# Kernel tuning notes

Measured on AMD Instinct MI355X. Metric: run time of the kernel, lower is better.

## Reference

```python
import jax, jax.numpy as jnp
import numpy as np

K_HOPS = 2  # SGConv K = nlayers


def setup_inputs() -> dict:
    key = jax.random.key(0)
    k1, k2, k3 = jax.random.split(key, 3)
    N, E, F, C = 100000, 1600000, 128, 40
    x = jax.random.normal(k1, (N, F), dtype=jnp.float32)
    edge_index = jax.random.randint(k2, (2, E), 0, N, dtype=jnp.int64)
    W = jax.random.normal(k3, (C, F), dtype=jnp.float32) * (1.0 / np.sqrt(F))
    b = jnp.zeros((C,), dtype=jnp.float32)
    return {"x": x, "edge_index": edge_index, "W": W, "b": b}


def reference(x, edge_index, W, b):
    # SGConv: K hops of GCN-normalized propagation (with self-loops), then Linear.
    N = x.shape[0]
    loop = jnp.arange(N, dtype=edge_index.dtype)
    src = jnp.concatenate([edge_index[0], loop])  # message source
    dst = jnp.concatenate([edge_index[1], loop])  # aggregation target
    w = jnp.ones(src.shape[0], dtype=x.dtype)     # edge_weight=None -> 1, self-loop fill=1
    deg = jax.ops.segment_sum(w, dst, num_segments=N)  # in-degree incl. self-loop (>=1)
    dinv = jax.lax.rsqrt(deg)
    norm = dinv[src] * w * dinv[dst]              # D^{-1/2} A D^{-1/2}
    h = x
    for _ in range(K_HOPS):
        h = jax.ops.segment_sum(norm[:, None] * h[src], dst, num_segments=N)
    return h @ W.T + b
```

## Files before the change

### kernel.cpp

```cpp
#include <hip/hip_runtime.h>
#include <hip/hip_fp16.h>
#include <cstdint>

#define CDIM 40
#define FDIM 128
#define BIN_SHIFT 8
#define BIN_SZ (1 << BIN_SHIFT)
#define CHUNK 4096
#define STAGE_CAP 8192

typedef _Float16 f16x8 __attribute__((ext_vector_type(8)));
typedef float f32x4 __attribute__((ext_vector_type(4)));

static __device__ __forceinline__ long long load_idx(const void* p, int is64, long long i) {
    if (is64) return ((const long long*)p)[i];
    return (long long)((const int*)p)[i];
}

static __device__ __forceinline__ unsigned packh2(float a, float b) {
    __half2 h;
    h.x = __float2half(a);
    h.y = __float2half(b);
    return *(unsigned*)&h;
}

static __device__ __forceinline__ void addv(float* acc, uint4 v) {
    const __half2* h = (const __half2*)&v;
#pragma unroll
    for (int k = 0; k < 4; ++k) {
        float2 f = __half22float2(h[k]);
        acc[2 * k]     += f.x;
        acc[2 * k + 1] += f.y;
    }
}

static __device__ __forceinline__ f16x8 cvt8(float4 a, float4 b) {
    f16x8 r;
    r[0] = (_Float16)a.x; r[1] = (_Float16)a.y; r[2] = (_Float16)a.z; r[3] = (_Float16)a.w;
    r[4] = (_Float16)b.x; r[5] = (_Float16)b.y; r[6] = (_Float16)b.z; r[7] = (_Float16)b.w;
    return r;
}

__global__ void k_init(int* cursor, int nb, int cap) {
    int i = blockIdx.x * blockDim.x + threadIdx.x;
    if (i < nb) cursor[i] = i * cap;
}

__global__ __launch_bounds__(256) void kA3(const void* ei, long long E,
                                           int nb, int* __restrict__ cursor,
                                           unsigned* __restrict__ binned) {
    __shared__ unsigned lval[CHUNK];
    __shared__ unsigned short lbin[CHUNK];
    __shared__ int lcnt[512];
    __shared__ int lbase[512];
    __shared__ int lflag;
    int tid = threadIdx.x;
    if (tid == 0) lflag = 1;
    for (int i = tid; i < nb; i += 256) lcnt[i] = 0;
    __syncthreads();
    {
        const unsigned* w = (const unsigned*)ei;
        int nscan = (int)((2 * E < 4096) ? (2 * E) : 4096);
        for (int k = 1 + 2 * tid; k < nscan; k += 512)
            if (w[k] != 0u) lflag = 0;
    }
    __syncthreads();
    int is64 = lflag;
    long long base = (long long)blockIdx.x * CHUNK;
    int nk = (int)min((long long)CHUNK, E - base);
    for (int k = tid; k < nk; k += 256) {
        long long e = base + k;
        int s = (int)load_idx(ei, is64, e);
        int d = (int)load_idx(ei, is64, E + e);
        int bin = d >> BIN_SHIFT;
        lval[k] = (unsigned)s | ((unsigned)(d & (BIN_SZ - 1)) << 17);
        lbin[k] = (unsigned short)bin;
        atomicAdd(&lcnt[bin], 1);
    }
    __syncthreads();
    for (int i = tid; i < nb; i += 256) {
        int c = lcnt[i];
        lbase[i] = c ? atomicAdd(&cursor[i], c) : 0;
        lcnt[i] = 0;
    }
    __syncthreads();
    for (int k = tid; k < nk; k += 256) {
        int bin = lbin[k];
        int loc = atomicAdd(&lcnt[bin], 1);
        binned[lbase[bin] + loc] = lval[k];
    }
}

__global__ __launch_bounds__(256) void kB(const unsigned* __restrict__ binned,
                                          const int* __restrict__ cursor, int cap,
                                          int* __restrict__ rowp, int* __restrict__ rend,
                                          float* __restrict__ dinv,
                                          int* __restrict__ perm, int* __restrict__ cursorG,
                                          int* __restrict__ csr, int N) {
    __shared__ int lcnt[BIN_SZ];
    __shared__ int lexcl[BIN_SZ];
    __shared__ int ls[256];
    __shared__ int dh[64];
    __shared__ int stage[STAGE_CAP];
    int b = blockIdx.x, tid = threadIdx.x;
    int node0 = b << BIN_SHIFT;
    int nn = min(BIN_SZ, N - node0);
    int base = b * cap;
    int nedges = cursor[b] - base;

    lcnt[tid] = 0;
    if (tid < 64) dh[tid] = 0;
    __syncthreads();
    for (int t = tid; t < nedges; t += 256)
        atomicAdd(&lcnt[(binned[base + t] >> 17) & (BIN_SZ - 1)], 1);
    __syncthreads();
    int myc = lcnt[tid];
    ls[tid] = myc;
    __syncthreads();
    for (int off = 1; off < 256; off <<= 1) {
        int t = (tid >= off) ? ls[tid - off] : 0;
        __syncthreads();
        ls[tid] += t;
        __syncthreads();
    }
    int ex = ls[tid] - myc;
    lexcl[tid] = ex;
    if (tid < nn) {
        rowp[node0 + tid] = base + ex;
        rend[node0 + tid] = base + ex + myc;
        dinv[node0 + tid] = rsqrtf(1.0f + (float)myc);
        atomicAdd(&dh[min(myc, 63)], 1);
    }
    __syncthreads();
    int dv = (tid < 64) ? dh[tid] : 0;
    ls[tid] = dv;
    __syncthreads();
    for (int off = 1; off < 64; off <<= 1) {
        int t = (tid >= off) ? ls[tid - off] : 0;
        __syncthreads();
        ls[tid] += t;
        __syncthreads();
    }
    if (tid < 64) dh[tid] = ls[tid] - dv;
    __syncthreads();
    if (tid < nn) {
        int pos = atomicAdd(&dh[min(myc, 63)], 1);
        perm[node0 + pos] = node0 + tid;
    }
    __syncthreads();
    lcnt[tid] = lexcl[tid];
    __syncthreads();
    if (nedges <= STAGE_CAP) {
        for (int t = tid; t < nedges; t += 256) {
            unsigned v = binned[base + t];
            int src = (int)(v & 0x1FFFFu);
            int dl  = (int)((v >> 17) & (BIN_SZ - 1));
            int p = atomicAdd(&lcnt[dl], 1);
            stage[p] = src;
        }
        __syncthreads();
        for (int t = tid; t < nedges; t += 256) csr[base + t] = stage[t];
    } else {
        if (tid < nn) cursorG[node0 + tid] = base + lexcl[tid];
        __syncthreads();
        for (int t = tid; t < nedges; t += 256) {
            unsigned v = binned[base + t];
            int src = (int)(v & 0x1FFFFu);
            int dl  = (int)((v >> 17) & (BIN_SZ - 1));
            int p = atomicAdd(&cursorG[node0 + dl], 1);
            csr[p] = src;
        }
    }
}

__global__ __launch_bounds__(256) void k_gemm(const float* __restrict__ x,
                                              const float* __restrict__ W,
                                              const float* __restrict__ dinv,
                                              __half* __restrict__ gA,
                                              __half* __restrict__ gB, int N) {
    int wave = threadIdx.x >> 6;
    int lane = threadIdx.x & 63;
    int m = lane & 15;
    int quad = lane >> 4;
    f16x8 bfrag[3][4];
#pragma unroll
    for (int t = 0; t < 3; ++t) {
        int c = t * 16 + m;
#pragma unroll
        for (int q = 0; q < 4; ++q) {
            if (c < CDIM) {
                const float* wp = W + (size_t)c * FDIM + q * 32 + quad * 8;
                float4 w0 = *(const float4*)wp;
                float4 w1 = *(const float4*)(wp + 4);
                bfrag[t][q] = cvt8(w0, w1);
            } else {
                f16x8 z = {0, 0, 0, 0, 0, 0, 0, 0};
                bfrag[t][q] = z;
            }
        }
    }
#pragma unroll
    for (int i = 0; i < 4; ++i) {
        int nodebase = blockIdx.x * 256 + wave * 64 + i * 16;
        if (nodebase >= N) break;
        const float* xp = x + (size_t)(nodebase + m) * FDIM + quad * 8;
        f16x8 afrag[4];
#pragma unroll
        for (int q = 0; q < 4; ++q) {
            float4 x0 = *(const float4*)(xp + q * 32);
            float4 x1 = *(const float4*)(xp + q * 32 + 4);
            afrag[q] = cvt8(x0, x1);
        }
        f32x4 acc0 = {0, 0, 0, 0}, acc1 = {0, 0, 0, 0}, acc2 = {0, 0, 0, 0};
#pragma unroll
        for (int q = 0; q < 4; ++q) {
            acc0 = __builtin_amdgcn_mfma_f32_16x16x32_f16(afrag[q], bfrag[0][q], acc0, 0, 0, 0);
            acc1 = __builtin_amdgcn_mfma_f32_16x16x32_f16(afrag[q], bfrag[1][q], acc1, 0, 0, 0);
            acc2 = __builtin_amdgcn_mfma_f32_16x16x32_f16(afrag[q], bfrag[2][q], acc2, 0, 0, 0);
        }
        float4 dvv = *(const float4*)&dinv[nodebase + quad * 4];
        float ds[4] = {dvv.x, dvv.y, dvv.z, dvv.w};
#pragma unroll
        for (int r = 0; r < 4; ++r) {
            int node = nodebase + quad * 4 + r;
            gA[(size_t)node * 32 + m]      = __float2half(acc0[r] * ds[r]);
            gA[(size_t)node * 32 + 16 + m] = __float2half(acc1[r] * ds[r]);
            if (m < 8)
                gB[(size_t)node * 8 + m]   = __float2half(acc2[r] * ds[r]);
        }
    }
}

__global__ __launch_bounds__(256) void k_gather(const int* __restrict__ rowp,
                                                const int* __restrict__ rend,
                                                const int* __restrict__ csr,
                                                const int* __restrict__ perm,
                                                const float* __restrict__ dinv,
                                                const __half* __restrict__ gA,
                                                const __half* __restrict__ gB,
                                                const float* __restrict__ b,
                                                __half* __restrict__ goA,
                                                __half* __restrict__ goB,
                                                float* __restrict__ outF,
                                                int N, int mode) {
    unsigned t = blockIdx.x * 256 + threadIdx.x;
    unsigned gidx = t / 5, c = t - gidx * 5;
    if (gidx >= (unsigned)N) return;
    int node = perm[gidx];
    const uint4* src;
    unsigned stride;
    if (c < 4) { src = (const uint4*)gA + c; stride = 4; }
    else       { src = (const uint4*)gB;     stride = 1; }
    float acc[8];
#pragma unroll
    for (int i = 0; i < 8; ++i) acc[i] = 0.0f;
    addv(acc, src[(size_t)node * stride]);
    int j = rowp[node], end = rend[node];
    for (; j + 7 < end; j += 8) {
        int s0 = csr[j], s1 = csr[j + 1], s2 = csr[j + 2], s3 = csr[j + 3];
        int s4 = csr[j + 4], s5 = csr[j + 5], s6 = csr[j + 6], s7 = csr[j + 7];
        uint4 v0 = src[(size_t)s0 * stride];
        uint4 v1 = src[(size_t)s1 * stride];
        uint4 v2 = src[(size_t)s2 * stride];
        uint4 v3 = src[(size_t)s3 * stride];
        uint4 v4 = src[(size_t)s4 * stride];
        uint4 v5 = src[(size_t)s5 * stride];
        uint4 v6 = src[(size_t)s6 * stride];
        uint4 v7 = src[(size_t)s7 * stride];
        addv(acc, v0); addv(acc, v1); addv(acc, v2); addv(acc, v3);
        addv(acc, v4); addv(acc, v5); addv(acc, v6); addv(acc, v7);
    }
    for (; j + 1 < end; j += 2) {
        int s0 = csr[j], s1 = csr[j + 1];
        uint4 v0 = src[(size_t)s0 * stride];
        uint4 v1 = src[(size_t)s1 * stride];
        addv(acc, v0); addv(acc, v1);
    }
    if (j < end) addv(acc, src[(size_t)csr[j] * stride]);
    float d = dinv[node];
    if (mode == 0) {
        float s = d * d;
        uint4 o;
        unsigned* w = (unsigned*)&o;
#pragma unroll
        for (int k = 0; k < 4; ++k)
            w[k] = packh2(acc[2 * k] * s, acc[2 * k + 1] * s);
        if (c < 4) ((uint4*)goA)[(size_t)node * 4 + c] = o;
        else       ((uint4*)goB)[node] = o;
    } else {
        const float4* b4 = (const float4*)b + 2 * c;
        float4 bv0 = b4[0], bv1 = b4[1];
        float4 o0, o1;
        o0.x = acc[0] * d + bv0.x; o0.y = acc[1] * d + bv0.y;
        o0.z = acc[2] * d + bv0.z; o0.w = acc[3] * d + bv0.w;
        o1.x = acc[4] * d + bv1.x; o1.y = acc[5] * d + bv1.y;
        o1.z = acc[6] * d + bv1.z; o1.w = acc[7] * d + bv1.w;
        float4* op = (float4*)outF + (size_t)node * 10 + 2 * c;
        op[0] = o0;
        op[1] = o1;
    }
}

static inline size_t align256(size_t v) { return (v + 255) & ~(size_t)255; }

extern "C" void kernel_launch(void* const* d_in, const int* in_sizes, int n_in,
                              void* d_out, int out_size, void* d_ws, size_t ws_size,
                              hipStream_t stream) {
    const float* x  = (const float*)d_in[0];
    const void*  ei = d_in[1];
    const float* W  = (const float*)d_in[2];
    const float* b  = (const float*)d_in[3];
    float* out = (float*)d_out;

    const int N = in_sizes[0] / FDIM;
    const long long E = (long long)in_sizes[1] / 2;

    const int nb     = (N + BIN_SZ - 1) >> BIN_SHIFT;
    const int nchunk = (int)((E + CHUNK - 1) / CHUNK);
    int cap = (int)(E / nb) + 2048;
    if (cap > STAGE_CAP) cap = STAGE_CAP;

    char* wsb = (char*)d_ws;
    size_t off = 0;
    int*      cursor  = (int*)(wsb + off);      off = align256(off + (size_t)nb * 4);
    int*      rowp    = (int*)(wsb + off);      off = align256(off + (size_t)N * 4);
    int*      rend    = (int*)(wsb + off);      off = align256(off + (size_t)N * 4);
    int*      cursorG = (int*)(wsb + off);      off = align256(off + (size_t)N * 4);
    int*      perm    = (int*)(wsb + off);      off = align256(off + (size_t)N * 4);
    float*    dinv    = (float*)(wsb + off);    off = align256(off + (size_t)N * 4);
    __half*   gA0     = (__half*)(wsb + off);   off = align256(off + (size_t)N * 32 * 2);
    __half*   gB0     = (__half*)(wsb + off);   off = align256(off + (size_t)N * 8 * 2);
    __half*   gA1     = (__half*)(wsb + off);   off = align256(off + (size_t)N * 32 * 2);
    __half*   gB1     = (__half*)(wsb + off);   off = align256(off + (size_t)N * 8 * 2);
    unsigned* binned  = (unsigned*)(wsb + off); off = align256(off + (size_t)nb * cap * 4);
    int*      csr     = (int*)(wsb + off);      off = align256(off + (size_t)nb * cap * 4);

    const int B = 256;
    const int nbGE = (N + 255) / 256;
    const unsigned GT = 5u * (unsigned)N;
    const int nbGA = (int)((GT + B - 1) / B);

    k_init  <<<(nb + 255) / 256, 256, 0, stream>>>(cursor, nb, cap);
    kA3     <<<nchunk, B, 0, stream>>>(ei, E, nb, cursor, binned);
    kB      <<<nb, B, 0, stream>>>(binned, cursor, cap, rowp, rend, dinv, perm, cursorG, csr, N);
    k_gemm  <<<nbGE, B, 0, stream>>>(x, W, dinv, gA0, gB0, N);
    k_gather<<<nbGA, B, 0, stream>>>(rowp, rend, csr, perm, dinv, gA0, gB0, b,
                                     gA1, gB1, nullptr, N, 0);
    k_gather<<<nbGA, B, 0, stream>>>(rowp, rend, csr, perm, dinv, gA1, gB1, b,
                                     nullptr, nullptr, out, N, 1);
}
```

Baseline: 222.5 us.

## Pad CSR rows to multiples of four and pack per-node gather metadata

CSR rows are padded to a multiple of four with a sentinel index pointing at an added zero row in each feature buffer. This lets the gather loop use int4 index loads with no scalar tail. The separate rowp/rend/perm/dinv arrays are replaced by one int2 meta record per degree-sorted slot, holding row start, node id and degree, and the gather recomputes dinv from the degree. The cost is some wasted gathers of the zero row and a larger CSR allocation.

After: 215.6 us. 3.1% less time.

```diff
diff --git a/kernel.cpp b/kernel.cpp
--- a/kernel.cpp
+++ b/kernel.cpp
@@ -41,9 +41,9 @@
     return r;
 }
 
-__global__ void k_init(int* cursor, int nb, int cap) {
+__global__ void k_init(int* cursor, int nb, int capRec) {
     int i = blockIdx.x * blockDim.x + threadIdx.x;
-    if (i < nb) cursor[i] = i * cap;
+    if (i < nb) cursor[i] = i * capRec;
 }
 
 __global__ __launch_bounds__(256) void kA3(const void* ei, long long E,
@@ -92,30 +92,34 @@
 }
 
 __global__ __launch_bounds__(256) void kB(const unsigned* __restrict__ binned,
-                                          const int* __restrict__ cursor, int cap,
-                                          int* __restrict__ rowp, int* __restrict__ rend,
+                                          const int* __restrict__ cursor,
+                                          int capRec, int capC,
+                                          int2* __restrict__ meta,
                                           float* __restrict__ dinv,
-                                          int* __restrict__ perm, int* __restrict__ cursorG,
+                                          int* __restrict__ cursorG,
                                           int* __restrict__ csr, int N) {
     __shared__ int lcnt[BIN_SZ];
     __shared__ int lexcl[BIN_SZ];
     __shared__ int ls[256];
     __shared__ int dh[64];
+    __shared__ int tot;
     __shared__ int stage[STAGE_CAP];
     int b = blockIdx.x, tid = threadIdx.x;
     int node0 = b << BIN_SHIFT;
     int nn = min(BIN_SZ, N - node0);
-    int base = b * cap;
-    int nedges = cursor[b] - base;
+    int recBase = b * capRec;
+    int csrBase = b * capC;
+    int nedges = cursor[b] - recBase;
 
     lcnt[tid] = 0;
     if (tid < 64) dh[tid] = 0;
     __syncthreads();
     for (int t = tid; t < nedges; t += 256)
-        atomicAdd(&lcnt[(binned[base + t] >> 17) & (BIN_SZ - 1)], 1);
+        atomicAdd(&lcnt[(binned[recBase + t] >> 17) & (BIN_SZ - 1)], 1);
     __syncthreads();
     int myc = lcnt[tid];
-    ls[tid] = myc;
+    int psz = (myc + 3) & ~3;
+    ls[tid] = psz;
     __syncthreads();
     for (int off = 1; off < 256; off <<= 1) {
         int t = (tid >= off) ? ls[tid - off] : 0;
@@ -123,15 +127,15 @@
         ls[tid] += t;
         __syncthreads();
     }
-    int ex = ls[tid] - myc;
+    int ex = ls[tid] - psz;
     lexcl[tid] = ex;
+    if (tid == 255) tot = ls[255];
     if (tid < nn) {
-        rowp[node0 + tid] = base + ex;
-        rend[node0 + tid] = base + ex + myc;
         dinv[node0 + tid] = rsqrtf(1.0f + (float)myc);
         atomicAdd(&dh[min(myc, 63)], 1);
     }
     __syncthreads();
+    int total = tot;
     int dv = (tid < 64) ? dh[tid] : 0;
     ls[tid] = dv;
     __syncthreads();
@@ -145,31 +149,40 @@
     __syncthreads();
     if (tid < nn) {
         int pos = atomicAdd(&dh[min(myc, 63)], 1);
-        perm[node0 + pos] = node0 + tid;
-    }
-    __syncthreads();
-    lcnt[tid] = lexcl[tid];
-    __syncthreads();
-    if (nedges <= STAGE_CAP) {
+        int2 mi;
+        mi.x = csrBase + ex;
+        mi.y = (node0 + tid) | (myc << 17);
+        meta[node0 + pos] = mi;
+    }
+    __syncthreads();
+    lcnt[tid] = ex;
+    __syncthreads();
+    if (total <= STAGE_CAP) {
+        for (int t = tid; t < total; t += 256) stage[t] = N;
+        __syncthreads();
         for (int t = tid; t < nedges; t += 256) {
-            unsigned v = binned[base + t];
+            unsigned v = binned[recBase + t];
             int src = (int)(v & 0x1FFFFu);
             int dl  = (int)((v >> 17) & (BIN_SZ - 1));
             int p = atomicAdd(&lcnt[dl], 1);
             stage[p] = src;
         }
         __syncthreads();
-        for (int t = tid; t < nedges; t += 256) csr[base + t] = stage[t];
+        const int4* sp = (const int4*)stage;
+        int4* cp = (int4*)(csr + csrBase);
+        for (int t = tid; t < (total >> 2); t += 256) cp[t] = sp[t];
     } else {
-        if (tid < nn) cursorG[node0 + tid] = base + lexcl[tid];
+        if (tid < nn) cursorG[node0 + tid] = csrBase + ex;
         __syncthreads();
         for (int t = tid; t < nedges; t += 256) {
-            unsigned v = binned[base + t];
+            unsigned v = binned[recBase + t];
             int src = (int)(v & 0x1FFFFu);
             int dl  = (int)((v >> 17) & (BIN_SZ - 1));
             int p = atomicAdd(&cursorG[node0 + dl], 1);
             csr[p] = src;
         }
+        if (tid < nn)
+            for (int k = myc; k < psz; ++k) csr[csrBase + ex + k] = N;
     }
 }
 
@@ -178,6 +191,10 @@
                                               const float* __restrict__ dinv,
                                               __half* __restrict__ gA,
                                               __half* __restrict__ gB, int N) {
+    if (blockIdx.x == 0 && threadIdx.x < 20) {
+        if (threadIdx.x < 16) ((unsigned*)(gA + (size_t)N * 32))[threadIdx.x] = 0u;
+        else                  ((unsigned*)(gB + (size_t)N * 8))[threadIdx.x - 16] = 0u;
+    }
     int wave = threadIdx.x >> 6;
     int lane = threadIdx.x & 63;
     int m = lane & 15;
@@ -231,11 +248,8 @@
     }
 }
 
-__global__ __launch_bounds__(256) void k_gather(const int* __restrict__ rowp,
-                                                const int* __restrict__ rend,
+__global__ __launch_bounds__(256) void k_gather(const int2* __restrict__ meta,
                                                 const int* __restrict__ csr,
-                                                const int* __restrict__ perm,
-                                                const float* __restrict__ dinv,
                                                 const __half* __restrict__ gA,
                                                 const __half* __restrict__ gB,
                                                 const float* __restrict__ b,
@@ -244,9 +258,17 @@
                                                 float* __restrict__ outF,
                                                 int N, int mode) {
     unsigned t = blockIdx.x * 256 + threadIdx.x;
+    if (mode == 0 && t < 20) {
+        if (t < 16) ((unsigned*)(goA + (size_t)N * 32))[t] = 0u;
+        else        ((unsigned*)(goB + (size_t)N * 8))[t - 16] = 0u;
+    }
     unsigned gidx = t / 5, c = t - gidx * 5;
     if (gidx >= (unsigned)N) return;
-    int node = perm[gidx];
+    int2 mi = meta[gidx];
+    int j = mi.x;
+    int node = mi.y & 0x1FFFF;
+    int deg = mi.y >> 17;
+    int end_pad = j + ((deg + 3) & ~3);
     const uint4* src;
     unsigned stride;
     if (c < 4) { src = (const uint4*)gA + c; stride = 4; }
@@ -255,29 +277,29 @@
 #pragma unroll
     for (int i = 0; i < 8; ++i) acc[i] = 0.0f;
     addv(acc, src[(size_t)node * stride]);
-    int j = rowp[node], end = rend[node];
-    for (; j + 7 < end; j += 8) {
-        int s0 = csr[j], s1 = csr[j + 1], s2 = csr[j + 2], s3 = csr[j + 3];
-        int s4 = csr[j + 4], s5 = csr[j + 5], s6 = csr[j + 6], s7 = csr[j + 7];
-        uint4 v0 = src[(size_t)s0 * stride];
-        uint4 v1 = src[(size_t)s1 * stride];
-        uint4 v2 = src[(size_t)s2 * stride];
-        uint4 v3 = src[(size_t)s3 * stride];
-        uint4 v4 = src[(size_t)s4 * stride];
-        uint4 v5 = src[(size_t)s5 * stride];
-        uint4 v6 = src[(size_t)s6 * stride];
-        uint4 v7 = src[(size_t)s7 * stride];
+    for (; j + 8 <= end_pad; j += 8) {
+        int4 c0 = *(const int4*)&csr[j];
+        int4 c1 = *(const int4*)&csr[j + 4];
+        uint4 v0 = src[(size_t)c0.x * stride];
+        uint4 v1 = src[(size_t)c0.y * stride];
+        uint4 v2 = src[(size_t)c0.z * stride];
+        uint4 v3 = src[(size_t)c0.w * stride];
+        uint4 v4 = src[(size_t)c1.x * stride];
+        uint4 v5 = src[(size_t)c1.y * stride];
+        uint4 v6 = src[(size_t)c1.z * stride];
+        uint4 v7 = src[(size_t)c1.w * stride];
         addv(acc, v0); addv(acc, v1); addv(acc, v2); addv(acc, v3);
         addv(acc, v4); addv(acc, v5); addv(acc, v6); addv(acc, v7);
     }
-    for (; j + 1 < end; j += 2) {
-        int s0 = csr[j], s1 = csr[j + 1];
-        uint4 v0 = src[(size_t)s0 * stride];
-        uint4 v1 = src[(size_t)s1 * stride];
-        addv(acc, v0); addv(acc, v1);
-    }
-    if (j < end) addv(acc, src[(size_t)csr[j] * stride]);
-    float d = dinv[node];
+    if (j < end_pad) {
+        int4 c0 = *(const int4*)&csr[j];
+        uint4 v0 = src[(size_t)c0.x * stride];
+        uint4 v1 = src[(size_t)c0.y * stride];
+        uint4 v2 = src[(size_t)c0.z * stride];
+        uint4 v3 = src[(size_t)c0.w * stride];
+        addv(acc, v0); addv(acc, v1); addv(acc, v2); addv(acc, v3);
+    }
+    float d = rsqrtf(1.0f + (float)deg);
     if (mode == 0) {
         float s = d * d;
         uint4 o;
@@ -317,35 +339,32 @@
 
     const int nb     = (N + BIN_SZ - 1) >> BIN_SHIFT;
     const int nchunk = (int)((E + CHUNK - 1) / CHUNK);
-    int cap = (int)(E / nb) + 2048;
-    if (cap > STAGE_CAP) cap = STAGE_CAP;
+    int capRec = (int)(E / nb) + 2048;
+    if (capRec > STAGE_CAP) capRec = STAGE_CAP;
+    int capC = (capRec + BIN_SZ * 3 + 1027) & ~3;
 
     char* wsb = (char*)d_ws;
     size_t off = 0;
     int*      cursor  = (int*)(wsb + off);      off = align256(off + (size_t)nb * 4);
-    int*      rowp    = (int*)(wsb + off);      off = align256(off + (size_t)N * 4);
-    int*      rend    = (int*)(wsb + off);      off = align256(off + (size_t)N * 4);
     int*      cursorG = (int*)(wsb + off);      off = align256(off + (size_t)N * 4);
-    int*      perm    = (int*)(wsb + off);      off = align256(off + (size_t)N * 4);
+    int2*     meta    = (int2*)(wsb + off);     off = align256(off + (size_t)N * 8);
     float*    dinv    = (float*)(wsb + off);    off = align256(off + (size_t)N * 4);
-    __half*   gA0     = (__half*)(wsb + off);   off = align256(off + (size_t)N * 32 * 2);
-    __half*   gB0     = (__half*)(wsb + off);   off = align256(off + (size_t)N * 8 * 2);
-    __half*   gA1     = (__half*)(wsb + off);   off = align256(off + (size_t)N * 32 * 2);
-    __half*   gB1     = (__half*)(wsb + off);   off = align256(off + (size_t)N * 8 * 2);
-    unsigned* binned  = (unsigned*)(wsb + off); off = align256(off + (size_t)nb * cap * 4);
-    int*      csr     = (int*)(wsb + off);      off = align256(off + (size_t)nb * cap * 4);
+    __half*   gA0     = (__half*)(wsb + off);   off = align256(off + (size_t)(N + 1) * 32 * 2);
+    __half*   gB0     = (__half*)(wsb + off);   off = align256(off + (size_t)(N + 1) * 8 * 2);
+    __half*   gA1     = (__half*)(wsb + off);   off = align256(off + (size_t)(N + 1) * 32 * 2);
+    __half*   gB1     = (__half*)(wsb + off);   off = align256(off + (size_t)(N + 1) * 8 * 2);
+    unsigned* binned  = (unsigned*)(wsb + off); off = align256(off + (size_t)nb * capRec * 4);
+    int*      csr     = (int*)(wsb + off);      off = align256(off + (size_t)nb * capC * 4);
 
     const int B = 256;
     const int nbGE = (N + 255) / 256;
     const unsigned GT = 5u * (unsigned)N;
     const int nbGA = (int)((GT + B - 1) / B);
 
-    k_init  <<<(nb + 255) / 256, 256, 0, stream>>>(cursor, nb, cap);
+    k_init  <<<(nb + 255) / 256, 256, 0, stream>>>(cursor, nb, capRec);
     kA3     <<<nchunk, B, 0, stream>>>(ei, E, nb, cursor, binned);
-    kB      <<<nb, B, 0, stream>>>(binned, cursor, cap, rowp, rend, dinv, perm, cursorG, csr, N);
+    kB      <<<nb, B, 0, stream>>>(binned, cursor, capRec, capC, meta, dinv, cursorG, csr, N);
     k_gemm  <<<nbGE, B, 0, stream>>>(x, W, dinv, gA0, gB0, N);
-    k_gather<<<nbGA, B, 0, stream>>>(rowp, rend, csr, perm, dinv, gA0, gB0, b,
-                                     gA1, gB1, nullptr, N, 0);
-    k_gather<<<nbGA, B, 0, stream>>>(rowp, rend, csr, perm, dinv, gA1, gB1, b,
-                                     nullptr, nullptr, out, N, 1);
-}
+    k_gather<<<nbGA, B, 0, stream>>>(meta, csr, gA0, gB0, b, gA1, gB1, nullptr, N, 0);
+    k_gather<<<nbGA, B, 0, stream>>>(meta, csr, gA1, gB1, b, nullptr, nullptr, out, N, 1);
+}
```
